# Kernel optimization log

Measured on AMD Instinct MI355X. Metric: run time of the kernel, lower is better.

Reference implementation:

```python
import jax, jax.numpy as jnp
import numpy as np

N, K, D, GH = 19683, 26, 64, 32  # cells (27^3), max neighbors, state_size, gating hidden


def setup_inputs() -> dict:
    key = jax.random.key(0)
    ks = jax.random.split(key, 10)
    s = 0.1
    return {
        "current_state": jax.random.normal(ks[0], (N, D), jnp.float32),
        "neighbor_states": jax.random.normal(ks[1], (N, K, D), jnp.float32),
        "neighbor_cat": jax.random.randint(ks[2], (N, K), 0, 3),  # 0=local,1=functional,2=distant
        "W_local": s * jax.random.normal(ks[3], (2 * D, D), jnp.float32),
        "b_local": jnp.zeros((D,), jnp.float32),
        "W_f1": s * jax.random.normal(ks[4], (2 * D, 2 * D), jnp.float32),
        "b_f1": jnp.zeros((2 * D,), jnp.float32),
        "W_f2": s * jax.random.normal(ks[5], (2 * D, D), jnp.float32),
        "b_f2": jnp.zeros((D,), jnp.float32),
        "W_c1": s * jax.random.normal(ks[6], (2 * D, 2 * D), jnp.float32),
        "b_c1": jnp.zeros((2 * D,), jnp.float32),
        "W_c2": s * jax.random.normal(ks[7], (2 * D, D), jnp.float32),
        "b_c2": jnp.zeros((D,), jnp.float32),
        "W_g1": s * jax.random.normal(ks[8], (2 * D, GH), jnp.float32),
        "b_g1": jnp.zeros((GH,), jnp.float32),
        "W_g2": s * jax.random.normal(ks[9], (GH, 3), jnp.float32),
        "b_g2": jnp.zeros((3,), jnp.float32),
    }


def _masked_mean(nb, mask):
    # nb: [N,K,D], mask: [N,K] float -> mean over selected neighbors, count
    cnt = mask.sum(axis=1, keepdims=True)  # [N,1]
    mean = (nb * mask[..., None]).sum(axis=1) / jnp.maximum(cnt, 1.0)
    return mean, cnt


def reference(current_state, neighbor_states, neighbor_cat, W_local, b_local,
              W_f1, b_f1, W_f2, b_f2, W_c1, b_c1, W_c2, b_c2,
              W_g1, b_g1, W_g2, b_g2):
    cur, nb, cat = current_state, neighbor_states, neighbor_cat
    m_loc = (cat == 0).astype(cur.dtype)
    m_fun = (cat == 1).astype(cur.dtype)
    m_dst = (cat == 2).astype(cur.dtype)
    mean_l, cnt_l = _masked_mean(nb, m_loc)
    mean_f, cnt_f = _masked_mean(nb, m_fun)
    mean_d, cnt_d = _masked_mean(nb, m_dst)

    # local expert: SimpleLinear on [cur, local neighbor aggregate]
    out_l = jnp.tanh(jnp.concatenate([cur, mean_l], -1) @ W_local + b_local)
    out_l = jnp.where(cnt_l > 0, out_l, 0.0)  # zeros when no local neighbors

    # functional expert: HybridGNN-style 2-layer message MLP
    h = jnp.tanh(jnp.concatenate([cur, mean_f], -1) @ W_f1 + b_f1)
    out_f = jnp.tanh(h @ W_f2 + b_f2)
    out_f = jnp.where(cnt_f > 0, out_f, 0.0)

    # distant expert: lightweight CNF, 3 Euler integration steps
    x = cur
    dt = 1.0 / 3.0
    for _ in range(3):  # fixed integration_steps, not a data-dim loop
        v = jnp.tanh(jnp.concatenate([x, mean_d], -1) @ W_c1 + b_c1)
        x = x + dt * jnp.tanh(v @ W_c2 + b_c2)
    out_d = jnp.where(cnt_d > 0, x, 0.0)

    # gating network over [cur, neighbor_activity]
    act = nb.mean(axis=1)  # [N,D]
    g = jnp.tanh(jnp.concatenate([cur, act], -1) @ W_g1 + b_g1) @ W_g2 + b_g2
    w = jax.nn.softmax(g, axis=-1)  # [N,3]

    combined = w[:, 0:1] * out_l + w[:, 1:2] * out_f + w[:, 2:3] * out_d
    return combined, w
```

## Files before the change

kernel.cpp:

```cpp
#include <hip/hip_runtime.h>


#define NCELL 19683
#define KNB 26
#define NGRP 1231

typedef short bf16x8 __attribute__((ext_vector_type(8)));
typedef float f32x4 __attribute__((ext_vector_type(4)));

#define FB_L 0
#define FB_F1 16
#define FB_F2 48
#define FB_C1 64
#define FB_C2 96
#define FB_G1 112

__device__ __forceinline__ unsigned short f2b(float f) {
  unsigned u; __builtin_memcpy(&u, &f, 4);
  u += 0x7FFFu + ((u >> 16) & 1u);
  return (unsigned short)(u >> 16);
}
__device__ __forceinline__ unsigned pack2(float x, float y) {
  return (unsigned)f2b(x) | ((unsigned)f2b(y) << 16);
}
__device__ __forceinline__ float tanh_fast(float x) {
  float e = __expf(2.0f * x);
  return 1.0f - 2.0f * __builtin_amdgcn_rcpf(e + 1.0f);
}

__global__ __launch_bounds__(256) void k_repack(
    const float* __restrict__ Wl, const float* __restrict__ Wf1,
    const float* __restrict__ Wf2, const float* __restrict__ Wc1,
    const float* __restrict__ Wc2, const float* __restrict__ Wg1,
    char* __restrict__ ws) {
  int frag = blockIdx.x * 4 + (threadIdx.x >> 6);
  int lane = threadIdx.x & 63;
  if (frag >= 120) return;
  const float* src; int Nd, lf;
  if (frag < 16)       { src = Wl;  Nd = 64;  lf = frag; }
  else if (frag < 48)  { src = Wf1; Nd = 128; lf = frag - 16; }
  else if (frag < 64)  { src = Wf2; Nd = 64;  lf = frag - 48; }
  else if (frag < 96)  { src = Wc1; Nd = 128; lf = frag - 64; }
  else if (frag < 112) { src = Wc2; Nd = 64;  lf = frag - 96; }
  else                 { src = Wg1; Nd = 32;  lf = frag - 112; }
  int nt = lf >> 2, kt = lf & 3;
  int n = nt * 16 + (lane & 15);
  int k0 = kt * 32 + (lane >> 4) * 8;
  unsigned short o[8] __attribute__((aligned(16)));
#pragma unroll
  for (int j = 0; j < 8; j++) o[j] = f2b(src[(k0 + j) * Nd + n]);
  *(uint4*)(ws + ((size_t)frag * 64 + lane) * 16) = *(const uint4*)o;
}

__device__ __forceinline__ void afrags2(const uint4* lo, const uint4* hi, int m, int q, bf16x8* a) {
#pragma unroll
  for (int kt = 0; kt < 4; kt++) {
    const uint4* b = (kt < 2) ? lo : hi;
    int ch = ((kt & 1) * 4 + q) ^ (m & 7);
    a[kt] = *(const bf16x8*)&b[m * 8 + ch];
  }
}
__device__ __forceinline__ void afragsS(const uint4* sb, int m, int q, bf16x8* a) {
#pragma unroll
  for (int kt = 0; kt < 4; kt++) {
    int ch = (kt * 4 + q) ^ m;
    a[kt] = *(const bf16x8*)&sb[m * 16 + ch];
  }
}
template <int NT>
__device__ __forceinline__ void gemmN(const bf16x8* __restrict__ wf, int fb, const bf16x8* a,
                                      int lane, f32x4* out) {
#pragma unroll
  for (int nt = 0; nt < NT; nt++) {
    f32x4 acc = {0.f, 0.f, 0.f, 0.f};
#pragma unroll
    for (int kt = 0; kt < 4; kt++) {
      bf16x8 b = wf[(fb + nt * 4 + kt) * 64 + lane];
      acc = __builtin_amdgcn_mfma_f32_16x16x32_bf16(a[kt], b, acc, 0, 0, 0);
    }
    out[nt] = acc;
  }
}
__device__ __forceinline__ void store_sb(uint4* sb, int cell, int feat, float v) {
  ((unsigned short*)&sb[cell * 16 + ((feat >> 3) ^ cell)])[feat & 7] = f2b(v);
}
__device__ __forceinline__ void store_xb(uint4* xb, int cell, int feat, float v) {
  ((unsigned short*)&xb[cell * 8 + ((feat >> 3) ^ (cell & 7))])[feat & 7] = f2b(v);
}

__global__ __launch_bounds__(256, 4) void k_main(
    const float* __restrict__ curp, const float* __restrict__ nbp, const int* __restrict__ catp,
    const float* __restrict__ bl_, const float* __restrict__ bf1_, const float* __restrict__ bf2_,
    const float* __restrict__ bc1_, const float* __restrict__ bc2_, const float* __restrict__ bg1_,
    const float* __restrict__ Wg2, const float* __restrict__ bg2_,
    const char* __restrict__ ws, float* __restrict__ outp) {
  __shared__ uint4 smem[2080];
  uint4* curb = smem;
  uint4* mlb  = smem + 128;
  uint4* mfb  = smem + 256;
  uint4* mdb  = smem + 384;
  uint4* actb = smem + 512;
  uint4* xb   = smem + 640;
  uint4* sbF  = smem + 768;
  uint4* sbC  = smem + 1024;
  float* outL = (float*)(smem + 1280);
  float* outF = (float*)(smem + 1536);
  float* outD = (float*)(smem + 1792);
  float4* flagsb = (float4*)(smem + 2048);
  float4* wvalsb = (float4*)(smem + 2064);

  int tid = threadIdx.x, lane = tid & 63, wv = tid >> 6;
  int g = blockIdx.x;

  {
    int cq = lane >> 4, fq = lane & 15;
    int cellLoc = wv * 4 + cq;
    int cell = min(g * 16 + cellLoc, NCELL - 1);
    int c0 = catp[cell * KNB + fq];
    int c1 = (fq < KNB - 16) ? catp[cell * KNB + 16 + fq] : -1;
    unsigned long long B0a = __ballot(c0 == 0), B1a = __ballot(c0 == 1), B2a = __ballot(c0 == 2);
    unsigned long long B0b = __ballot(c1 == 0), B1b = __ballot(c1 == 1), B2b = __ballot(c1 == 2);
    int sh = cq * 16;
    unsigned m0 = (unsigned)((B0a >> sh) & 0xFFFFull) | ((unsigned)((B0b >> sh) & 0x3FFull) << 16);
    unsigned m1 = (unsigned)((B1a >> sh) & 0xFFFFull) | ((unsigned)((B1b >> sh) & 0x3FFull) << 16);
    unsigned m2 = (unsigned)((B2a >> sh) & 0xFFFFull) | ((unsigned)((B2b >> sh) & 0x3FFull) << 16);
    float cl = (float)__popc(m0), cf = (float)__popc(m1), cd = (float)__popc(m2);
    float sl[4] = {0, 0, 0, 0}, sf[4] = {0, 0, 0, 0}, sd[4] = {0, 0, 0, 0}, sa[4] = {0, 0, 0, 0};
    const float* nbc = nbp + (size_t)cell * (KNB * 64) + fq * 4;
#pragma unroll
    for (int k = 0; k < KNB; k++) {
      float4 v = *(const float4*)(nbc + k * 64);
      float b0 = (float)((m0 >> k) & 1u);
      float b1 = (float)((m1 >> k) & 1u);
      float b2 = (float)((m2 >> k) & 1u);
      sa[0] += v.x; sa[1] += v.y; sa[2] += v.z; sa[3] += v.w;
      sl[0] += b0 * v.x; sl[1] += b0 * v.y; sl[2] += b0 * v.z; sl[3] += b0 * v.w;
      sf[0] += b1 * v.x; sf[1] += b1 * v.y; sf[2] += b1 * v.z; sf[3] += b1 * v.w;
      sd[0] += b2 * v.x; sd[1] += b2 * v.y; sd[2] += b2 * v.z; sd[3] += b2 * v.w;
    }
    float rl = 1.0f / fmaxf(cl, 1.0f);
    float rf = 1.0f / fmaxf(cf, 1.0f);
    float rd = 1.0f / fmaxf(cd, 1.0f);
    const float r26 = 1.0f / 26.0f;
    int ch = (fq >> 1) ^ (cellLoc & 7);
    int sub = fq & 1;
    ((uint2*)&mlb[cellLoc * 8 + ch])[sub] =
        make_uint2(pack2(sl[0] * rl, sl[1] * rl), pack2(sl[2] * rl, sl[3] * rl));
    ((uint2*)&mfb[cellLoc * 8 + ch])[sub] =
        make_uint2(pack2(sf[0] * rf, sf[1] * rf), pack2(sf[2] * rf, sf[3] * rf));
    ((uint2*)&mdb[cellLoc * 8 + ch])[sub] =
        make_uint2(pack2(sd[0] * rd, sd[1] * rd), pack2(sd[2] * rd, sd[3] * rd));
    ((uint2*)&actb[cellLoc * 8 + ch])[sub] =
        make_uint2(pack2(sa[0] * r26, sa[1] * r26), pack2(sa[2] * r26, sa[3] * r26));
    if (fq == 0)
      flagsb[cellLoc] = make_float4(cl > 0.f ? 1.f : 0.f, cf > 0.f ? 1.f : 0.f,
                                    cd > 0.f ? 1.f : 0.f, 0.f);
  }
  if (tid < 128) {
    int cellLoc = tid >> 3, c = tid & 7;
    int cell = min(g * 16 + cellLoc, NCELL - 1);
    const float4* cp = (const float4*)(curp + (size_t)cell * 64) + c * 2;
    float4 A = cp[0], B = cp[1];
    uint4 o;
    o.x = pack2(A.x, A.y); o.y = pack2(A.z, A.w);
    o.z = pack2(B.x, B.y); o.w = pack2(B.z, B.w);
    curb[cellLoc * 8 + (c ^ (cellLoc & 7))] = o;
  }

  int m = lane & 15, q = lane >> 4;
  const bf16x8* wf = (const bf16x8*)ws;
  bf16x8 a4[4];
  float xr[2][4];

  if (wv >= 2) {
    int ntb = (wv - 2) * 2;
#pragma unroll
    for (int j = 0; j < 2; j++)
#pragma unroll
      for (int r = 0; r < 4; r++) {
        int cell = min(g * 16 + q * 4 + r, NCELL - 1);
        xr[j][r] = curp[(size_t)cell * 64 + (ntb + j) * 16 + m];
      }
  }
  __syncthreads();

  if (wv == 0) {
    afrags2(curb, mlb, m, q, a4);
    f32x4 ol[4];
    gemmN<4>(wf, FB_L, a4, lane, ol);
#pragma unroll
    for (int nt = 0; nt < 4; nt++) {
      float bb = bl_[nt * 16 + m];
#pragma unroll
      for (int r = 0; r < 4; r++) outL[(q * 4 + r) * 64 + nt * 16 + m] = tanh_fast(ol[nt][r] + bb);
    }
    afrags2(curb, actb, m, q, a4);
    f32x4 gh[2];
    gemmN<2>(wf, FB_G1, a4, lane, gh);
#pragma unroll
    for (int nt = 0; nt < 2; nt++) {
      float bb = bg1_[nt * 16 + m];
#pragma unroll
      for (int r = 0; r < 4; r++) gh[nt][r] = tanh_fast(gh[nt][r] + bb);
    }
    float w2v[2][3];
#pragma unroll
    for (int nt = 0; nt < 2; nt++)
#pragma unroll
      for (int t = 0; t < 3; t++) w2v[nt][t] = Wg2[(nt * 16 + m) * 3 + t];
    float bg2v[3] = {bg2_[0], bg2_[1], bg2_[2]};
#pragma unroll
    for (int r = 0; r < 4; r++) {
      float gv[3];
#pragma unroll
      for (int t = 0; t < 3; t++) {
        float p = gh[0][r] * w2v[0][t] + gh[1][r] * w2v[1][t];
        p += __shfl_xor(p, 1); p += __shfl_xor(p, 2); p += __shfl_xor(p, 4); p += __shfl_xor(p, 8);
        gv[t] = p + bg2v[t];
      }
      float mx = fmaxf(gv[0], fmaxf(gv[1], gv[2]));
      float e0 = __expf(gv[0] - mx), e1 = __expf(gv[1] - mx), e2 = __expf(gv[2] - mx);
      float rs = __builtin_amdgcn_rcpf(e0 + e1 + e2);
      int cellLoc = q * 4 + r;
      int cell = g * 16 + cellLoc;
      if (m == 0) wvalsb[cellLoc] = make_float4(e0 * rs, e1 * rs, e2 * rs, 0.f);
      if (cell < NCELL && m < 3) {
        float wsel = (m == 0) ? e0 * rs : (m == 1) ? e1 * rs : e2 * rs;
        outp[(size_t)NCELL * 64 + cell * 3 + m] = wsel;
      }
    }
  } else if (wv == 1) {
    afrags2(curb, mfb, m, q, a4);
    f32x4 h8[8];
    gemmN<8>(wf, FB_F1, a4, lane, h8);
#pragma unroll
    for (int nt = 0; nt < 8; nt++) {
      float bb = bf1_[nt * 16 + m];
#pragma unroll
      for (int r = 0; r < 4; r++)
        store_sb(sbF, q * 4 + r, nt * 16 + m, tanh_fast(h8[nt][r] + bb));
    }
    afragsS(sbF, m, q, a4);
    f32x4 of4[4];
    gemmN<4>(wf, FB_F2, a4, lane, of4);
#pragma unroll
    for (int nt = 0; nt < 4; nt++) {
      float bb = bf2_[nt * 16 + m];
#pragma unroll
      for (int r = 0; r < 4; r++)
        outF[(q * 4 + r) * 64 + nt * 16 + m] = tanh_fast(of4[nt][r] + bb);
    }
  } else {
    int ntb = (wv - 2) * 2;
#pragma unroll
    for (int j = 0; j < 2; j++)
#pragma unroll
      for (int r = 0; r < 4; r++) store_xb(xb, q * 4 + r, (ntb + j) * 16 + m, xr[j][r]);
  }

  for (int step = 0; step < 3; step++) {
    __syncthreads();
    if (wv >= 2) {
      int hb = (wv - 2) * 4;
      afrags2(xb, mdb, m, q, a4);
      f32x4 v4[4];
      gemmN<4>(wf, FB_C1 + hb * 4, a4, lane, v4);
#pragma unroll
      for (int j = 0; j < 4; j++) {
        int nt = hb + j;
        float bb = bc1_[nt * 16 + m];
#pragma unroll
        for (int r = 0; r < 4; r++)
          store_sb(sbC, q * 4 + r, nt * 16 + m, tanh_fast(v4[j][r] + bb));
      }
    }
    __syncthreads();
    if (wv >= 2) {
      int ntb = (wv - 2) * 2;
      afragsS(sbC, m, q, a4);
      f32x4 dx2[2];
      gemmN<2>(wf, FB_C2 + ntb * 4, a4, lane, dx2);
#pragma unroll
      for (int j = 0; j < 2; j++) {
        int nt = ntb + j;
        float bb = bc2_[nt * 16 + m];
#pragma unroll
        for (int r = 0; r < 4; r++) {
          xr[j][r] += (1.0f / 3.0f) * tanh_fast(dx2[j][r] + bb);
          if (step < 2) store_xb(xb, q * 4 + r, nt * 16 + m, xr[j][r]);
          else outD[(q * 4 + r) * 64 + nt * 16 + m] = xr[j][r];
        }
      }
    }
  }
  __syncthreads();

  {
    int cellLoc = tid >> 4, fi = tid & 15;
    float4 vl = ((const float4*)outL)[cellLoc * 16 + fi];
    float4 vf = ((const float4*)outF)[cellLoc * 16 + fi];
    float4 vd = ((const float4*)outD)[cellLoc * 16 + fi];
    float4 fl = flagsb[cellLoc];
    float4 wv4 = wvalsb[cellLoc];
    float a0 = wv4.x * fl.x, a1 = wv4.y * fl.y, a2 = wv4.z * fl.z;
    int cell = g * 16 + cellLoc;
    if (cell < NCELL) {
      float4 res;
      res.x = a0 * vl.x + a1 * vf.x + a2 * vd.x;
      res.y = a0 * vl.y + a1 * vf.y + a2 * vd.y;
      res.z = a0 * vl.z + a1 * vf.z + a2 * vd.z;
      res.w = a0 * vl.w + a1 * vf.w + a2 * vd.w;
      ((float4*)(outp + (size_t)cell * 64))[fi] = res;
    }
  }
}

extern "C" void kernel_launch(void* const* d_in, const int* in_sizes, int n_in,
                              void* d_out, int out_size, void* d_ws, size_t ws_size,
                              hipStream_t stream) {
  const float* cur = (const float*)d_in[0];
  const float* nb  = (const float*)d_in[1];
  const int* cat   = (const int*)d_in[2];
  const float* Wl  = (const float*)d_in[3];
  const float* bl  = (const float*)d_in[4];
  const float* Wf1 = (const float*)d_in[5];
  const float* bf1 = (const float*)d_in[6];
  const float* Wf2 = (const float*)d_in[7];
  const float* bf2 = (const float*)d_in[8];
  const float* Wc1 = (const float*)d_in[9];
  const float* bc1 = (const float*)d_in[10];
  const float* Wc2 = (const float*)d_in[11];
  const float* bc2 = (const float*)d_in[12];
  const float* Wg1 = (const float*)d_in[13];
  const float* bg1 = (const float*)d_in[14];
  const float* Wg2 = (const float*)d_in[15];
  const float* bg2 = (const float*)d_in[16];
  char* ws = (char*)d_ws;
  float* outp = (float*)d_out;

  k_repack<<<30, 256, 0, stream>>>(Wl, Wf1, Wf2, Wc1, Wc2, Wg1, ws);
  k_main<<<NGRP, 256, 0, stream>>>(cur, nb, cat, bl, bf1, bf2, bc1, bc2, bg1, Wg2, bg2,
                                   (const char*)ws, outp);
}
```

Measured before the change: 248.7 us.

## Shrink LDS footprint with bf16 expert outputs and raise occupancy to 6 blocks

Expert outputs are staged in shared memory as bf16 instead of fp32, and the functional and CNF hidden buffers share a single scratch region. This cuts LDS per block from about 33KB to 23KB, and the launch bound is raised to 6 blocks per CU so more waves can hide the latency of the memory-bound neighbor reads. The neighbor reduction now issues loads in batches of 9 float4 before accumulating, and the all-neighbor mean is derived from the three category sums rather than kept as a separate accumulator. The cost is extra bf16 rounding on the final outputs, and a tighter register budget that may cause spills.

```diff
diff --git a/kernel.cpp b/kernel.cpp
--- a/kernel.cpp
+++ b/kernel.cpp
@@ -19,6 +19,9 @@
   unsigned u; __builtin_memcpy(&u, &f, 4);
   u += 0x7FFFu + ((u >> 16) & 1u);
   return (unsigned short)(u >> 16);
+}
+__device__ __forceinline__ float b2f(unsigned short h) {
+  unsigned u = ((unsigned)h) << 16; float f; __builtin_memcpy(&f, &u, 4); return f;
 }
 __device__ __forceinline__ unsigned pack2(float x, float y) {
   return (unsigned)f2b(x) | ((unsigned)f2b(y) << 16);
@@ -88,26 +91,25 @@
   ((unsigned short*)&xb[cell * 8 + ((feat >> 3) ^ (cell & 7))])[feat & 7] = f2b(v);
 }
 
-__global__ __launch_bounds__(256, 4) void k_main(
+__global__ __launch_bounds__(256, 6) void k_main(
     const float* __restrict__ curp, const float* __restrict__ nbp, const int* __restrict__ catp,
     const float* __restrict__ bl_, const float* __restrict__ bf1_, const float* __restrict__ bf2_,
     const float* __restrict__ bc1_, const float* __restrict__ bc2_, const float* __restrict__ bg1_,
     const float* __restrict__ Wg2, const float* __restrict__ bg2_,
     const char* __restrict__ ws, float* __restrict__ outp) {
-  __shared__ uint4 smem[2080];
+  __shared__ uint4 smem[1440];
   uint4* curb = smem;
   uint4* mlb  = smem + 128;
   uint4* mfb  = smem + 256;
   uint4* mdb  = smem + 384;
   uint4* actb = smem + 512;
   uint4* xb   = smem + 640;
-  uint4* sbF  = smem + 768;
-  uint4* sbC  = smem + 1024;
-  float* outL = (float*)(smem + 1280);
-  float* outF = (float*)(smem + 1536);
-  float* outD = (float*)(smem + 1792);
-  float4* flagsb = (float4*)(smem + 2048);
-  float4* wvalsb = (float4*)(smem + 2064);
+  uint4* sbS  = smem + 768;
+  unsigned short* outLh = (unsigned short*)(smem + 1024);
+  unsigned short* outFh = (unsigned short*)(smem + 1152);
+  unsigned short* outDh = (unsigned short*)(smem + 1280);
+  float4* flagsb = (float4*)(smem + 1408);
+  float4* wvalsb = (float4*)(smem + 1424);
 
   int tid = threadIdx.x, lane = tid & 63, wv = tid >> 6;
   int g = blockIdx.x;
@@ -125,18 +127,27 @@
     unsigned m1 = (unsigned)((B1a >> sh) & 0xFFFFull) | ((unsigned)((B1b >> sh) & 0x3FFull) << 16);
     unsigned m2 = (unsigned)((B2a >> sh) & 0xFFFFull) | ((unsigned)((B2b >> sh) & 0x3FFull) << 16);
     float cl = (float)__popc(m0), cf = (float)__popc(m1), cd = (float)__popc(m2);
-    float sl[4] = {0, 0, 0, 0}, sf[4] = {0, 0, 0, 0}, sd[4] = {0, 0, 0, 0}, sa[4] = {0, 0, 0, 0};
+    float sl[4] = {0, 0, 0, 0}, sf[4] = {0, 0, 0, 0}, sd[4] = {0, 0, 0, 0};
     const float* nbc = nbp + (size_t)cell * (KNB * 64) + fq * 4;
 #pragma unroll
-    for (int k = 0; k < KNB; k++) {
-      float4 v = *(const float4*)(nbc + k * 64);
-      float b0 = (float)((m0 >> k) & 1u);
-      float b1 = (float)((m1 >> k) & 1u);
-      float b2 = (float)((m2 >> k) & 1u);
-      sa[0] += v.x; sa[1] += v.y; sa[2] += v.z; sa[3] += v.w;
-      sl[0] += b0 * v.x; sl[1] += b0 * v.y; sl[2] += b0 * v.z; sl[3] += b0 * v.w;
-      sf[0] += b1 * v.x; sf[1] += b1 * v.y; sf[2] += b1 * v.z; sf[3] += b1 * v.w;
-      sd[0] += b2 * v.x; sd[1] += b2 * v.y; sd[2] += b2 * v.z; sd[3] += b2 * v.w;
+    for (int b = 0; b < 3; b++) {
+      const int k0 = b * 9;
+      const int kn = (b == 2) ? 8 : 9;
+      float4 v[9];
+#pragma unroll
+      for (int k = 0; k < 9; k++)
+        if (k < kn) v[k] = *(const float4*)(nbc + (k0 + k) * 64);
+#pragma unroll
+      for (int k = 0; k < 9; k++) {
+        if (k >= kn) break;
+        int kk = k0 + k;
+        float b0 = (float)((m0 >> kk) & 1u);
+        float b1 = (float)((m1 >> kk) & 1u);
+        float b2 = (float)((m2 >> kk) & 1u);
+        sl[0] += b0 * v[k].x; sl[1] += b0 * v[k].y; sl[2] += b0 * v[k].z; sl[3] += b0 * v[k].w;
+        sf[0] += b1 * v[k].x; sf[1] += b1 * v[k].y; sf[2] += b1 * v[k].z; sf[3] += b1 * v[k].w;
+        sd[0] += b2 * v[k].x; sd[1] += b2 * v[k].y; sd[2] += b2 * v[k].z; sd[3] += b2 * v[k].w;
+      }
     }
     float rl = 1.0f / fmaxf(cl, 1.0f);
     float rf = 1.0f / fmaxf(cf, 1.0f);
@@ -151,7 +162,8 @@
     ((uint2*)&mdb[cellLoc * 8 + ch])[sub] =
         make_uint2(pack2(sd[0] * rd, sd[1] * rd), pack2(sd[2] * rd, sd[3] * rd));
     ((uint2*)&actb[cellLoc * 8 + ch])[sub] =
-        make_uint2(pack2(sa[0] * r26, sa[1] * r26), pack2(sa[2] * r26, sa[3] * r26));
+        make_uint2(pack2((sl[0] + sf[0] + sd[0]) * r26, (sl[1] + sf[1] + sd[1]) * r26),
+                   pack2((sl[2] + sf[2] + sd[2]) * r26, (sl[3] + sf[3] + sd[3]) * r26));
     if (fq == 0)
       flagsb[cellLoc] = make_float4(cl > 0.f ? 1.f : 0.f, cf > 0.f ? 1.f : 0.f,
                                     cd > 0.f ? 1.f : 0.f, 0.f);
@@ -192,7 +204,8 @@
     for (int nt = 0; nt < 4; nt++) {
       float bb = bl_[nt * 16 + m];
 #pragma unroll
-      for (int r = 0; r < 4; r++) outL[(q * 4 + r) * 64 + nt * 16 + m] = tanh_fast(ol[nt][r] + bb);
+      for (int r = 0; r < 4; r++)
+        outLh[(q * 4 + r) * 64 + nt * 16 + m] = f2b(tanh_fast(ol[nt][r] + bb));
     }
     afrags2(curb, actb, m, q, a4);
     f32x4 gh[2];
@@ -238,9 +251,9 @@
       float bb = bf1_[nt * 16 + m];
 #pragma unroll
       for (int r = 0; r < 4; r++)
-        store_sb(sbF, q * 4 + r, nt * 16 + m, tanh_fast(h8[nt][r] + bb));
-    }
-    afragsS(sbF, m, q, a4);
+        store_sb(sbS, q * 4 + r, nt * 16 + m, tanh_fast(h8[nt][r] + bb));
+    }
+    afragsS(sbS, m, q, a4);
     f32x4 of4[4];
     gemmN<4>(wf, FB_F2, a4, lane, of4);
 #pragma unroll
@@ -248,7 +261,7 @@
       float bb = bf2_[nt * 16 + m];
 #pragma unroll
       for (int r = 0; r < 4; r++)
-        outF[(q * 4 + r) * 64 + nt * 16 + m] = tanh_fast(of4[nt][r] + bb);
+        outFh[(q * 4 + r) * 64 + nt * 16 + m] = f2b(tanh_fast(of4[nt][r] + bb));
     }
   } else {
     int ntb = (wv - 2) * 2;
@@ -271,13 +284,13 @@
         float bb = bc1_[nt * 16 + m];
 #pragma unroll
         for (int r = 0; r < 4; r++)
-          store_sb(sbC, q * 4 + r, nt * 16 + m, tanh_fast(v4[j][r] + bb));
+          store_sb(sbS, q * 4 + r, nt * 16 + m, tanh_fast(v4[j][r] + bb));
       }
     }
     __syncthreads();
     if (wv >= 2) {
       int ntb = (wv - 2) * 2;
-      afragsS(sbC, m, q, a4);
+      afragsS(sbS, m, q, a4);
       f32x4 dx2[2];
       gemmN<2>(wf, FB_C2 + ntb * 4, a4, lane, dx2);
 #pragma unroll
@@ -288,7 +301,7 @@
         for (int r = 0; r < 4; r++) {
           xr[j][r] += (1.0f / 3.0f) * tanh_fast(dx2[j][r] + bb);
           if (step < 2) store_xb(xb, q * 4 + r, nt * 16 + m, xr[j][r]);
-          else outD[(q * 4 + r) * 64 + nt * 16 + m] = xr[j][r];
+          else outDh[(q * 4 + r) * 64 + nt * 16 + m] = f2b(xr[j][r]);
         }
       }
     }
@@ -297,19 +310,23 @@
 
   {
     int cellLoc = tid >> 4, fi = tid & 15;
-    float4 vl = ((const float4*)outL)[cellLoc * 16 + fi];
-    float4 vf = ((const float4*)outF)[cellLoc * 16 + fi];
-    float4 vd = ((const float4*)outD)[cellLoc * 16 + fi];
+    uint2 ul = ((const uint2*)outLh)[cellLoc * 16 + fi];
+    uint2 uf = ((const uint2*)outFh)[cellLoc * 16 + fi];
+    uint2 ud = ((const uint2*)outDh)[cellLoc * 16 + fi];
     float4 fl = flagsb[cellLoc];
     float4 wv4 = wvalsb[cellLoc];
     float a0 = wv4.x * fl.x, a1 = wv4.y * fl.y, a2 = wv4.z * fl.z;
     int cell = g * 16 + cellLoc;
     if (cell < NCELL) {
       float4 res;
-      res.x = a0 * vl.x + a1 * vf.x + a2 * vd.x;
-      res.y = a0 * vl.y + a1 * vf.y + a2 * vd.y;
-      res.z = a0 * vl.z + a1 * vf.z + a2 * vd.z;
-      res.w = a0 * vl.w + a1 * vf.w + a2 * vd.w;
+      res.x = a0 * b2f((unsigned short)ul.x) + a1 * b2f((unsigned short)uf.x) +
+              a2 * b2f((unsigned short)ud.x);
+      res.y = a0 * b2f((unsigned short)(ul.x >> 16)) + a1 * b2f((unsigned short)(uf.x >> 16)) +
+              a2 * b2f((unsigned short)(ud.x >> 16));
+      res.z = a0 * b2f((unsigned short)ul.y) + a1 * b2f((unsigned short)uf.y) +
+              a2 * b2f((unsigned short)ud.y);
+      res.w = a0 * b2f((unsigned short)(ul.y >> 16)) + a1 * b2f((unsigned short)(uf.y >> 16)) +
+              a2 * b2f((unsigned short)(ud.y >> 16));
       ((float4*)(outp + (size_t)cell * 64))[fi] = res;
     }
   }
```

Result: slower. 266.3 us (+7.1%).
